# Performance work log

Hardware: AMD Instinct MI355X
Metric: run time of the kernel (lower is better)

## Reference

```python
import jax, jax.numpy as jnp
import numpy as np

B, S, C = 64, 256, 512
H, O, L = 1024, 1024, 4


def setup_inputs() -> dict:
    key = jax.random.key(0)
    ks = jax.random.split(key, 8)
    inp = {
        "x": jax.random.normal(ks[0], (B, S, C), dtype=jnp.float32),
        "hid_layer": jax.random.normal(ks[1], (B, L, H), dtype=jnp.float32),
        "fc1_w": jax.random.normal(ks[2], (H, H + C), dtype=jnp.float32) * (1.0 / np.sqrt(H + C)),
        "fc1_b": jax.random.normal(ks[3], (H,), dtype=jnp.float32) * 0.01,
        "fc2_w": jax.random.normal(ks[4], (O, H), dtype=jnp.float32) * (1.0 / np.sqrt(H)),
        "fc2_b": jax.random.normal(ks[5], (O,), dtype=jnp.float32) * 0.01,
        "lin_w": jax.random.normal(ks[6], (L - 1, H, H), dtype=jnp.float32) * (1.0 / np.sqrt(H)),
        "lin_b": jax.random.normal(ks[7], (L - 1, H), dtype=jnp.float32) * 0.01,
    }
    return inp


def reference(x, hid_layer, fc1_w, fc1_b, fc2_w, fc2_b, lin_w, lin_b):
    # x: [B,S,C] -> [S,B,C]; hid_layer: [B,L,H] -> [L,B,H]
    xs = jnp.transpose(x, (1, 0, 2))
    h = jnp.transpose(hid_layer, (1, 0, 2))
    h0 = h[0]          # layer-0 hidden: never updated in original code (constant)
    h_rest = h[1:]     # [L-1, B, H], evolves by repeated affine map
    n_inner = lin_w.shape[0]

    def step(carry, x_i):
        hr = carry  # [L-1, B, H]
        # hid_layer[i+1, j+1] = linears[j](hid_layer[i, j+1])
        h_new = jnp.einsum("lbh,lgh->lbg", hr, lin_w) + lin_b[:, None, :]
        xc = jnp.concatenate([x_i, h0], axis=1)            # [B, C+H]
        temp = jnp.tanh(xc @ fc1_w.T + fc1_b)              # [B, H]
        for j in range(n_inner):                           # static small loop
            temp = jnp.tanh(h_new[j] + temp)
        out = jax.nn.softmax(jax.nn.relu(temp @ fc2_w.T + fc2_b), axis=-1)
        return h_new, out

    _, outs = jax.lax.scan(step, h_rest, xs)
    return outs  # [S, B, O]
```

## Files before the change

### kernel.cpp

```cpp
#include <hip/hip_runtime.h>
#include <hip/hip_bf16.h>

#define Bn 64
#define Sn 256
#define Cn 512
#define Hn 1024
#define On 1024
#define NL 3

__global__ __launch_bounds__(256) void prep_kernel(const float* __restrict__ hid,
                                                   float* __restrict__ h0T) {
    __shared__ float T[64][65];
    int l = blockIdx.x >> 4;
    int kb = (blockIdx.x & 15) * 64;
    int tid = threadIdx.x;
    for (int e = tid; e < 1024; e += 256) {
        int b = e >> 4, k4 = (e & 15) * 4;
        float4 v = *(const float4*)&hid[(size_t)b * 4096 + (size_t)(l + 1) * 1024 + kb + k4];
        T[b][k4] = v.x; T[b][k4 + 1] = v.y; T[b][k4 + 2] = v.z; T[b][k4 + 3] = v.w;
    }
    __syncthreads();
    for (int e = tid; e < 1024; e += 256) {
        int k = e >> 4, b4 = (e & 15) * 4;
        float4 v = make_float4(T[b4][k], T[b4 + 1][k], T[b4 + 2][k], T[b4 + 3][k]);
        *(float4*)&h0T[(size_t)l * 65536 + (size_t)(kb + k) * 64 + b4] = v;
    }
}

__global__ __launch_bounds__(256) void g1_kernel(const float* __restrict__ hid,
                                                 const float* __restrict__ fc1_w,
                                                 const float* __restrict__ fc1_b,
                                                 float* __restrict__ h0proj) {
    __shared__ __align__(16) float h0s[Hn];
    int b = blockIdx.x;
    int tid = threadIdx.x;
    for (int i = tid; i < Hn; i += 256) h0s[i] = hid[(size_t)b * 4 * Hn + i];
    __syncthreads();
    for (int g = tid; g < Hn; g += 256) {
        const float* wr = fc1_w + (size_t)g * (Cn + Hn) + Cn;
        float acc = 0.f;
        for (int k = 0; k < Hn; k += 4) {
            float4 w4 = *(const float4*)&wr[k];
            acc = fmaf(w4.x, h0s[k + 0], acc);
            acc = fmaf(w4.y, h0s[k + 1], acc);
            acc = fmaf(w4.z, h0s[k + 2], acc);
            acc = fmaf(w4.w, h0s[k + 3], acc);
        }
        h0proj[b * Hn + g] = acc + fc1_b[g];
    }
}

__global__ __launch_bounds__(256) void g2_kernel(const float* __restrict__ x,
                                                 const float* __restrict__ fc1_w,
                                                 const float* __restrict__ h0proj,
                                                 __hip_bfloat16* __restrict__ tb) {
    __shared__ __align__(16) float As[64][64];
    __shared__ __align__(16) float Bs[64][64];
    int tid = threadIdx.x;
    int bx = blockIdx.x;
    int g0 = blockIdx.y * 64;
    int ml = tid & 63;
    int kq = tid >> 6;
    const float* xrow = x + (size_t)ml * (Sn * Cn) + (size_t)bx * Cn;
    const float* wrow = fc1_w + (size_t)(g0 + ml) * (Cn + Hn);
    int wave = tid >> 6, lane = tid & 63;
    int tm = (wave & 1) * 32 + (lane & 7) * 4;
    int tg = (wave >> 1) * 32 + (lane >> 3) * 4;
    float acc[4][4] = {};
    for (int kc = 0; kc < Cn / 64; ++kc) {
#pragma unroll
        for (int r = 0; r < 4; ++r) {
            int kk = kq * 16 + r * 4;
            float4 v = *(const float4*)&xrow[kc * 64 + kk];
            As[kk + 0][ml] = v.x; As[kk + 1][ml] = v.y;
            As[kk + 2][ml] = v.z; As[kk + 3][ml] = v.w;
        }
#pragma unroll
        for (int r = 0; r < 4; ++r) {
            int kk = kq * 16 + r * 4;
            float4 v = *(const float4*)&wrow[kc * 64 + kk];
            Bs[kk + 0][ml] = v.x; Bs[kk + 1][ml] = v.y;
            Bs[kk + 2][ml] = v.z; Bs[kk + 3][ml] = v.w;
        }
        __syncthreads();
#pragma unroll 4
        for (int k = 0; k < 64; ++k) {
            float4 a4 = *(const float4*)&As[k][tm];
            float4 b4 = *(const float4*)&Bs[k][tg];
            float av[4] = {a4.x, a4.y, a4.z, a4.w};
            float bv[4] = {b4.x, b4.y, b4.z, b4.w};
#pragma unroll
            for (int i = 0; i < 4; ++i)
#pragma unroll
                for (int j = 0; j < 4; ++j)
                    acc[i][j] = fmaf(av[i], bv[j], acc[i][j]);
        }
        __syncthreads();
    }
#pragma unroll
    for (int j = 0; j < 4; ++j) {
        int g = g0 + tg + j;
        union { ushort4 u4; __hip_bfloat16 h[4]; } cv;
#pragma unroll
        for (int i = 0; i < 4; ++i) {
            float hp = h0proj[(size_t)(tm + i) * Hn + g];
            cv.h[i] = __float2bfloat16(tanhf(acc[i][j] + hp));
        }
        *(ushort4*)&tb[((size_t)bx * Hn + g) * 64 + tm] = cv.u4;
    }
}

__global__ __launch_bounds__(256) void g3_kernel(const __hip_bfloat16* __restrict__ tb,
                                                 const float* __restrict__ fc2_w,
                                                 const float* __restrict__ fc2_b,
                                                 float* __restrict__ logits) {
    __shared__ __align__(16) float As[64][64];
    __shared__ __align__(16) float Bs[64][64];
    int tid = threadIdx.x;
    int bx = blockIdx.x;
    int g0 = blockIdx.y * 64;
    int ml = tid & 63;
    int kq = tid >> 6;
    const float* wrow = fc2_w + (size_t)(g0 + ml) * Hn;
    int wave = tid >> 6, lane = tid & 63;
    int tm = (wave & 1) * 32 + (lane & 7) * 4;
    int tg = (wave >> 1) * 32 + (lane >> 3) * 4;
    float acc[4][4] = {};
    for (int kc = 0; kc < Hn / 64; ++kc) {
        for (int e = tid; e < 4096; e += 256) {
            int kk = e >> 6, mm = e & 63;
            As[kk][mm] = __bfloat162float(tb[((size_t)bx * Hn + kc * 64 + kk) * 64 + mm]);
        }
#pragma unroll
        for (int r = 0; r < 4; ++r) {
            int kk = kq * 16 + r * 4;
            float4 v = *(const float4*)&wrow[kc * 64 + kk];
            Bs[kk + 0][ml] = v.x; Bs[kk + 1][ml] = v.y;
            Bs[kk + 2][ml] = v.z; Bs[kk + 3][ml] = v.w;
        }
        __syncthreads();
#pragma unroll 4
        for (int k = 0; k < 64; ++k) {
            float4 a4 = *(const float4*)&As[k][tm];
            float4 b4 = *(const float4*)&Bs[k][tg];
            float av[4] = {a4.x, a4.y, a4.z, a4.w};
            float bv[4] = {b4.x, b4.y, b4.z, b4.w};
#pragma unroll
            for (int i = 0; i < 4; ++i)
#pragma unroll
                for (int j = 0; j < 4; ++j)
                    acc[i][j] = fmaf(av[i], bv[j], acc[i][j]);
        }
        __syncthreads();
    }
    int m0 = bx * 64;
#pragma unroll
    for (int i = 0; i < 4; ++i) {
        int m = m0 + tm + i;
        float4 o;
        o.x = fmaxf(acc[i][0] + fc2_b[g0 + tg + 0], 0.f);
        o.y = fmaxf(acc[i][1] + fc2_b[g0 + tg + 1], 0.f);
        o.z = fmaxf(acc[i][2] + fc2_b[g0 + tg + 2], 0.f);
        o.w = fmaxf(acc[i][3] + fc2_b[g0 + tg + 3], 0.f);
        *(float4*)&logits[(size_t)m * Hn + g0 + tg] = o;
    }
}

__global__ __launch_bounds__(256) void cvec_kernel(const float* __restrict__ A,
                                                   const float* __restrict__ vecB,
                                                   const float* __restrict__ addB,
                                                   float* __restrict__ outv) {
    int row = blockIdx.x * 4 + (threadIdx.x >> 6);
    int lane = threadIdx.x & 63;
    int l = row >> 10;
    const float* ar = A + (size_t)row * Hn;
    const float* vb = vecB + (size_t)l * Hn;
    float s = 0.f;
#pragma unroll 4
    for (int j = 0; j < 16; ++j) {
        int k = lane + j * 64;
        s = fmaf(ar[k], vb[k], s);
    }
    s += __shfl_xor(s, 1);  s += __shfl_xor(s, 2);  s += __shfl_xor(s, 4);
    s += __shfl_xor(s, 8);  s += __shfl_xor(s, 16); s += __shfl_xor(s, 32);
    if (lane == 0) outv[row] = s + addB[row];
}

template<int NC>
__global__ __launch_bounds__(512, 2) void gsl4_kernel(
        const float* __restrict__ A,
        const float* __restrict__ Bsrc,
        unsigned long long bPanel, int bstride, int bcol0,
        float* __restrict__ dst, int dstride, int dcol0,
        const float* __restrict__ addRow,
        __hip_bfloat16* __restrict__ tb, const float* __restrict__ Xf,
        int folds, int do_gemm) {
    __shared__ __align__(16) float As[2][16][16];
    __shared__ __align__(16) float Xs[2][16][NC];
    const int tid = threadIdx.x;
    const int wg = blockIdx.x;
    const int row0 = wg * 16;
    const int l = row0 >> 10;

    if (folds >= 0) {
        for (int e = wg * 512 + tid; e < 4 * Hn * Bn; e += 192 * 512) {
            int b = e & 63, g = (e >> 6) & 1023, tp = e >> 16;
            int c = tp * 64 + b;
            size_t tix = ((size_t)(4 * folds + tp) * Hn + g) * 64 + b;
            float tv = __bfloat162float(tb[tix]);
            tv = tanhf(Xf[(size_t)g * 256 + c] + tv);
            tv = tanhf(Xf[262144 + (size_t)g * 256 + c] + tv);
            tv = tanhf(Xf[524288 + (size_t)g * 256 + c] + tv);
            tb[tix] = __float2bfloat16(tv);
        }
    }
    if (!do_gemm) return;

    const int cq = tid & 127;
    const int rq = tid >> 7;
    const float* __restrict__ Bp = Bsrc + (size_t)l * bPanel + bcol0;
    constexpr int NF4 = NC / 4;
    constexpr int TOT4 = 16 * NF4;
    constexpr int PFN = (TOT4 + 511) / 512;
    const bool cact = (2 * cq < NC);
    const int arow = tid & 15, akq = tid >> 4;
    const bool aact = (tid < 64);

    float acc[4][2] = {};
    float4 px[PFN];
    float4 pa;

#pragma unroll
    for (int i = 0; i < PFN; ++i) {
        int e = tid + i * 512;
        if ((TOT4 % 512 == 0) || e < TOT4) {
            int k = e / NF4, c4 = (e % NF4) * 4;
            px[i] = *(const float4*)(Bp + (size_t)k * bstride + c4);
        }
    }
    if (aact)
        pa = *(const float4*)(A + (size_t)(row0 + arow) * 1024 + akq * 4);
#pragma unroll
    for (int i = 0; i < PFN; ++i) {
        int e = tid + i * 512;
        if ((TOT4 % 512 == 0) || e < TOT4) {
            int k = e / NF4, c4 = (e % NF4) * 4;
            *(float4*)&Xs[0][k][c4] = px[i];
        }
    }
    if (aact) {
        As[0][akq * 4 + 0][arow] = pa.x;
        As[0][akq * 4 + 1][arow] = pa.y;
        As[0][akq * 4 + 2][arow] = pa.z;
        As[0][akq * 4 + 3][arow] = pa.w;
    }
    __syncthreads();

    for (int ck = 0; ck < 64; ++ck) {
        if (ck < 63) {
#pragma unroll
            for (int i = 0; i < PFN; ++i) {
                int e = tid + i * 512;
                if ((TOT4 % 512 == 0) || e < TOT4) {
                    int k = e / NF4, c4 = (e % NF4) * 4;
                    px[i] = *(const float4*)(Bp + (size_t)((ck + 1) * 16 + k) * bstride + c4);
                }
            }
            if (aact)
                pa = *(const float4*)(A + (size_t)(row0 + arow) * 1024 + (ck + 1) * 16 + akq * 4);
        }
        if (cact) {
            const float* xsc = &Xs[ck & 1][0][2 * cq];
            const float* asc = &As[ck & 1][0][rq * 4];
#pragma unroll
            for (int kk = 0; kk < 16; ++kk) {
                float4 a4 = *(const float4*)(asc + kk * 16);
                float2 x2 = *(const float2*)(xsc + kk * NC);
                acc[0][0] = fmaf(a4.x, x2.x, acc[0][0]);
                acc[0][1] = fmaf(a4.x, x2.y, acc[0][1]);
                acc[1][0] = fmaf(a4.y, x2.x, acc[1][0]);
                acc[1][1] = fmaf(a4.y, x2.y, acc[1][1]);
                acc[2][0] = fmaf(a4.z, x2.x, acc[2][0]);
                acc[2][1] = fmaf(a4.z, x2.y, acc[2][1]);
                acc[3][0] = fmaf(a4.w, x2.x, acc[3][0]);
                acc[3][1] = fmaf(a4.w, x2.y, acc[3][1]);
            }
        }
        if (ck < 63) {
#pragma unroll
            for (int i = 0; i < PFN; ++i) {
                int e = tid + i * 512;
                if ((TOT4 % 512 == 0) || e < TOT4) {
                    int k = e / NF4, c4 = (e % NF4) * 4;
                    *(float4*)&Xs[(ck + 1) & 1][k][c4] = px[i];
                }
            }
            if (aact) {
                As[(ck + 1) & 1][akq * 4 + 0][arow] = pa.x;
                As[(ck + 1) & 1][akq * 4 + 1][arow] = pa.y;
                As[(ck + 1) & 1][akq * 4 + 2][arow] = pa.z;
                As[(ck + 1) & 1][akq * 4 + 3][arow] = pa.w;
            }
            __syncthreads();
        }
    }

    if (cact) {
#pragma unroll
        for (int i = 0; i < 4; ++i) {
            int r = row0 + rq * 4 + i;
            float av = addRow ? addRow[r] : 0.0f;
            float2 o = make_float2(acc[i][0] + av, acc[i][1] + av);
            *(float2*)(dst + (size_t)r * dstride + dcol0 + 2 * cq) = o;
        }
    }
}

__global__ __launch_bounds__(256) void softmax_kernel(const float* __restrict__ logits,
                                                      float* __restrict__ out) {
    __shared__ float redm[4];
    __shared__ float reds[4];
    __shared__ float bcast[2];
    int row = blockIdx.x, tid = threadIdx.x;
    const float* in = logits + (size_t)row * On;
    float4 v = *(const float4*)&in[tid * 4];
    float mx = fmaxf(fmaxf(v.x, v.y), fmaxf(v.z, v.w));
#pragma unroll
    for (int o = 32; o > 0; o >>= 1) mx = fmaxf(mx, __shfl_down(mx, o));
    if ((tid & 63) == 0) redm[tid >> 6] = mx;
    __syncthreads();
    if (tid == 0) bcast[0] = fmaxf(fmaxf(redm[0], redm[1]), fmaxf(redm[2], redm[3]));
    __syncthreads();
    float M = bcast[0];
    float e0 = expf(v.x - M), e1 = expf(v.y - M), e2 = expf(v.z - M), e3 = expf(v.w - M);
    float s = e0 + e1 + e2 + e3;
#pragma unroll
    for (int o = 32; o > 0; o >>= 1) s += __shfl_down(s, o);
    if ((tid & 63) == 0) reds[tid >> 6] = s;
    __syncthreads();
    if (tid == 0) bcast[1] = reds[0] + reds[1] + reds[2] + reds[3];
    __syncthreads();
    float inv = 1.0f / bcast[1];
    float4 o4 = make_float4(e0 * inv, e1 * inv, e2 * inv, e3 * inv);
    *(float4*)&out[(size_t)row * On + tid * 4] = o4;
}

extern "C" void kernel_launch(void* const* d_in, const int* in_sizes, int n_in,
                              void* d_out, int out_size, void* d_ws, size_t ws_size,
                              hipStream_t stream) {
    const float* x     = (const float*)d_in[0];
    const float* hid   = (const float*)d_in[1];
    const float* fc1_w = (const float*)d_in[2];
    const float* fc1_b = (const float*)d_in[3];
    const float* fc2_w = (const float*)d_in[4];
    const float* fc2_b = (const float*)d_in[5];
    const float* lin_w = (const float*)d_in[6];
    const float* lin_b = (const float*)d_in[7];
    float* out = (float*)d_out;

    char* wsb = (char*)d_ws;
    __hip_bfloat16* tb = (__hip_bfloat16*)wsb;
    float* logits = (float*)(wsb + 33554432ull);
    float* w2     = (float*)(wsb + 100663296ull);
    float* w4     = (float*)(wsb + 113246208ull);
    float* X      = (float*)(wsb + 125829120ull);
    float* c2     = (float*)(wsb + 132120576ull);
    float* c4     = (float*)(wsb + 132132864ull);
    float* h0T    = (float*)(wsb + 132145152ull);
    float* h0proj = (float*)(wsb + 132931584ull);

    float* X0 = X;
    float* X1 = X + 786432;

    prep_kernel<<<48, 256, 0, stream>>>(hid, h0T);
    g1_kernel<<<Bn, 256, 0, stream>>>(hid, fc1_w, fc1_b, h0proj);
    g2_kernel<<<dim3(Sn, Hn / 64), 256, 0, stream>>>(x, fc1_w, h0proj, tb);

    cvec_kernel<<<768, 256, 0, stream>>>(lin_w, lin_b, lin_b, c2);
    for (int p = 0; p < 4; ++p)
        gsl4_kernel<256><<<192, 512, 0, stream>>>(lin_w, lin_w, 1048576ull, 1024, p * 256,
                                                  w2, 1024, p * 256, nullptr,
                                                  tb, nullptr, -1, 1);
    cvec_kernel<<<768, 256, 0, stream>>>(w2, c2, c2, c4);
    for (int p = 0; p < 4; ++p)
        gsl4_kernel<256><<<192, 512, 0, stream>>>(w2, w2, 1048576ull, 1024, p * 256,
                                                  w4, 1024, p * 256, nullptr,
                                                  tb, nullptr, -1, 1);
    gsl4_kernel<64><<<192, 512, 0, stream>>>(lin_w, h0T, 65536ull, 64, 0,
                                             X0, 256, 0, lin_b, tb, nullptr, -1, 1);
    gsl4_kernel<64><<<192, 512, 0, stream>>>(w2, h0T, 65536ull, 64, 0,
                                             X0, 256, 64, c2, tb, nullptr, -1, 1);
    gsl4_kernel<64><<<192, 512, 0, stream>>>(w4, h0T, 65536ull, 64, 0,
                                             X0, 256, 192, c4, tb, nullptr, -1, 1);
    gsl4_kernel<64><<<192, 512, 0, stream>>>(w2, X0, 262144ull, 256, 0,
                                             X0, 256, 128, c2, tb, nullptr, -1, 1);

    for (int s = 0; s < 63; ++s) {
        float* Xin  = (s & 1) ? X1 : X0;
        float* Xout = (s & 1) ? X0 : X1;
        gsl4_kernel<256><<<192, 512, 0, stream>>>(w4, Xin, 262144ull, 256, 0,
                                                  Xout, 256, 0, c4, tb, Xin, s, 1);
    }
    gsl4_kernel<256><<<192, 512, 0, stream>>>(w4, X1, 262144ull, 256, 0,
                                              X0, 256, 0, c4, tb, X1, 63, 0);

    g3_kernel<<<dim3(Sn, Hn / 64), 256, 0, stream>>>(tb, fc2_w, fc2_b, logits);
    softmax_kernel<<<Sn * Bn, 256, 0, stream>>>(logits, out);
}
```

Measured before the change: 5.034 ms.

## Fuse recurrence launches into one cooperative persistent kernel with grid syncs

The precompute GEMMs (W², W⁴, bias vectors, initial X panels) and the 63-step recurrence loop are merged into one cooperatively launched kernel of 192 blocks, with grid.sync between dependent phases. This replaces roughly eighty separate kernel launches and their launch gaps. The GEMM inner loop now uses two register prefetch buffers so loads run two chunks ahead instead of one. The cvec reduction is folded in per block. In exchange, grid-wide barriers now carry the dependencies, and every block must stay resident for the whole run.

```diff
diff --git a/kernel.cpp b/kernel.cpp
--- a/kernel.cpp
+++ b/kernel.cpp
@@ -1,5 +1,8 @@
 #include <hip/hip_runtime.h>
 #include <hip/hip_bf16.h>
+#include <hip/hip_cooperative_groups.h>
+
+namespace cg = cooperative_groups;
 
 #define Bn 64
 #define Sn 256
@@ -166,154 +169,177 @@
     }
 }
 
-__global__ __launch_bounds__(256) void cvec_kernel(const float* __restrict__ A,
-                                                   const float* __restrict__ vecB,
-                                                   const float* __restrict__ addB,
-                                                   float* __restrict__ outv) {
-    int row = blockIdx.x * 4 + (threadIdx.x >> 6);
-    int lane = threadIdx.x & 63;
-    int l = row >> 10;
-    const float* ar = A + (size_t)row * Hn;
-    const float* vb = vecB + (size_t)l * Hn;
-    float s = 0.f;
-#pragma unroll 4
-    for (int j = 0; j < 16; ++j) {
-        int k = lane + j * 64;
-        s = fmaf(ar[k], vb[k], s);
-    }
-    s += __shfl_xor(s, 1);  s += __shfl_xor(s, 2);  s += __shfl_xor(s, 4);
-    s += __shfl_xor(s, 8);  s += __shfl_xor(s, 16); s += __shfl_xor(s, 32);
-    if (lane == 0) outv[row] = s + addB[row];
-}
-
 template<int NC>
-__global__ __launch_bounds__(512, 2) void gsl4_kernel(
-        const float* __restrict__ A,
-        const float* __restrict__ Bsrc,
-        unsigned long long bPanel, int bstride, int bcol0,
+__device__ __forceinline__ void gemm_pass(
+        const float* __restrict__ A, int row0,
+        const float* __restrict__ Bp, int bstride,
         float* __restrict__ dst, int dstride, int dcol0,
-        const float* __restrict__ addRow,
-        __hip_bfloat16* __restrict__ tb, const float* __restrict__ Xf,
-        int folds, int do_gemm) {
-    __shared__ __align__(16) float As[2][16][16];
-    __shared__ __align__(16) float Xs[2][16][NC];
-    const int tid = threadIdx.x;
-    const int wg = blockIdx.x;
-    const int row0 = wg * 16;
-    const int l = row0 >> 10;
-
-    if (folds >= 0) {
-        for (int e = wg * 512 + tid; e < 4 * Hn * Bn; e += 192 * 512) {
-            int b = e & 63, g = (e >> 6) & 1023, tp = e >> 16;
-            int c = tp * 64 + b;
-            size_t tix = ((size_t)(4 * folds + tp) * Hn + g) * 64 + b;
-            float tv = __bfloat162float(tb[tix]);
-            tv = tanhf(Xf[(size_t)g * 256 + c] + tv);
-            tv = tanhf(Xf[262144 + (size_t)g * 256 + c] + tv);
-            tv = tanhf(Xf[524288 + (size_t)g * 256 + c] + tv);
-            tb[tix] = __float2bfloat16(tv);
-        }
-    }
-    if (!do_gemm) return;
-
-    const int cq = tid & 127;
-    const int rq = tid >> 7;
-    const float* __restrict__ Bp = Bsrc + (size_t)l * bPanel + bcol0;
+        const float* __restrict__ addRow, int tid,
+        float* __restrict__ AsF, float* __restrict__ XsF) {
     constexpr int NF4 = NC / 4;
     constexpr int TOT4 = 16 * NF4;
     constexpr int PFN = (TOT4 + 511) / 512;
+    const int cq = tid & 127;
+    const int rq = tid >> 7;
     const bool cact = (2 * cq < NC);
     const int arow = tid & 15, akq = tid >> 4;
     const bool aact = (tid < 64);
 
     float acc[4][2] = {};
-    float4 px[PFN];
-    float4 pa;
-
-#pragma unroll
-    for (int i = 0; i < PFN; ++i) {
-        int e = tid + i * 512;
-        if ((TOT4 % 512 == 0) || e < TOT4) {
-            int k = e / NF4, c4 = (e % NF4) * 4;
-            px[i] = *(const float4*)(Bp + (size_t)k * bstride + c4);
-        }
-    }
-    if (aact)
-        pa = *(const float4*)(A + (size_t)(row0 + arow) * 1024 + akq * 4);
-#pragma unroll
-    for (int i = 0; i < PFN; ++i) {
-        int e = tid + i * 512;
-        if ((TOT4 % 512 == 0) || e < TOT4) {
-            int k = e / NF4, c4 = (e % NF4) * 4;
-            *(float4*)&Xs[0][k][c4] = px[i];
-        }
-    }
-    if (aact) {
-        As[0][akq * 4 + 0][arow] = pa.x;
-        As[0][akq * 4 + 1][arow] = pa.y;
-        As[0][akq * 4 + 2][arow] = pa.z;
-        As[0][akq * 4 + 3][arow] = pa.w;
-    }
-    __syncthreads();
-
-    for (int ck = 0; ck < 64; ++ck) {
-        if (ck < 63) {
-#pragma unroll
-            for (int i = 0; i < PFN; ++i) {
-                int e = tid + i * 512;
-                if ((TOT4 % 512 == 0) || e < TOT4) {
-                    int k = e / NF4, c4 = (e % NF4) * 4;
-                    px[i] = *(const float4*)(Bp + (size_t)((ck + 1) * 16 + k) * bstride + c4);
-                }
+    float4 pxA[PFN], pxB[PFN], paA = {}, paB = {};
+
+    auto loadX = [&](int c, float4* px) {
+#pragma unroll
+        for (int i = 0; i < PFN; ++i) {
+            int e = tid + i * 512;
+            if ((TOT4 % 512 == 0) || e < TOT4) {
+                int k = e / NF4, c4 = (e % NF4) * 4;
+                px[i] = *(const float4*)(Bp + (size_t)(c * 16 + k) * bstride + c4);
             }
-            if (aact)
-                pa = *(const float4*)(A + (size_t)(row0 + arow) * 1024 + (ck + 1) * 16 + akq * 4);
-        }
-        if (cact) {
-            const float* xsc = &Xs[ck & 1][0][2 * cq];
-            const float* asc = &As[ck & 1][0][rq * 4];
-#pragma unroll
-            for (int kk = 0; kk < 16; ++kk) {
-                float4 a4 = *(const float4*)(asc + kk * 16);
-                float2 x2 = *(const float2*)(xsc + kk * NC);
-                acc[0][0] = fmaf(a4.x, x2.x, acc[0][0]);
-                acc[0][1] = fmaf(a4.x, x2.y, acc[0][1]);
-                acc[1][0] = fmaf(a4.y, x2.x, acc[1][0]);
-                acc[1][1] = fmaf(a4.y, x2.y, acc[1][1]);
-                acc[2][0] = fmaf(a4.z, x2.x, acc[2][0]);
-                acc[2][1] = fmaf(a4.z, x2.y, acc[2][1]);
-                acc[3][0] = fmaf(a4.w, x2.x, acc[3][0]);
-                acc[3][1] = fmaf(a4.w, x2.y, acc[3][1]);
+        }
+    };
+    auto writeX = [&](int c, const float4* px) {
+#pragma unroll
+        for (int i = 0; i < PFN; ++i) {
+            int e = tid + i * 512;
+            if ((TOT4 % 512 == 0) || e < TOT4) {
+                int k = e / NF4, c4 = (e % NF4) * 4;
+                *(float4*)&XsF[(size_t)(c & 1) * 4096 + k * 256 + c4] = px[i];
             }
         }
-        if (ck < 63) {
-#pragma unroll
-            for (int i = 0; i < PFN; ++i) {
-                int e = tid + i * 512;
-                if ((TOT4 % 512 == 0) || e < TOT4) {
-                    int k = e / NF4, c4 = (e % NF4) * 4;
-                    *(float4*)&Xs[(ck + 1) & 1][k][c4] = px[i];
-                }
-            }
-            if (aact) {
-                As[(ck + 1) & 1][akq * 4 + 0][arow] = pa.x;
-                As[(ck + 1) & 1][akq * 4 + 1][arow] = pa.y;
-                As[(ck + 1) & 1][akq * 4 + 2][arow] = pa.z;
-                As[(ck + 1) & 1][akq * 4 + 3][arow] = pa.w;
-            }
+    };
+    auto loadA = [&](int c) -> float4 {
+        return *(const float4*)(A + (size_t)(row0 + arow) * 1024 + c * 16 + akq * 4);
+    };
+    auto writeA = [&](int c, float4 pa) {
+        float* base = &AsF[(size_t)(c & 1) * 256 + arow];
+        base[(akq * 4 + 0) * 16] = pa.x;
+        base[(akq * 4 + 1) * 16] = pa.y;
+        base[(akq * 4 + 2) * 16] = pa.z;
+        base[(akq * 4 + 3) * 16] = pa.w;
+    };
+    auto compute = [&](int c) {
+        if (!cact) return;
+        const float* xsc = &XsF[(size_t)(c & 1) * 4096 + 2 * cq];
+        const float* asc = &AsF[(size_t)(c & 1) * 256 + rq * 4];
+#pragma unroll
+        for (int kk = 0; kk < 16; ++kk) {
+            float4 a4 = *(const float4*)(asc + kk * 16);
+            float2 x2 = *(const float2*)(xsc + kk * 256);
+            acc[0][0] = fmaf(a4.x, x2.x, acc[0][0]);
+            acc[0][1] = fmaf(a4.x, x2.y, acc[0][1]);
+            acc[1][0] = fmaf(a4.y, x2.x, acc[1][0]);
+            acc[1][1] = fmaf(a4.y, x2.y, acc[1][1]);
+            acc[2][0] = fmaf(a4.z, x2.x, acc[2][0]);
+            acc[2][1] = fmaf(a4.z, x2.y, acc[2][1]);
+            acc[3][0] = fmaf(a4.w, x2.x, acc[3][0]);
+            acc[3][1] = fmaf(a4.w, x2.y, acc[3][1]);
+        }
+    };
+
+    loadX(0, pxA); if (aact) paA = loadA(0);
+    loadX(1, pxB); if (aact) paB = loadA(1);
+    writeX(0, pxA); if (aact) writeA(0, paA);
+    __syncthreads();
+    for (int c2i = 0; c2i < 32; ++c2i) {
+        const int ck = 2 * c2i;
+        if (ck + 2 < 64) { loadX(ck + 2, pxA); if (aact) paA = loadA(ck + 2); }
+        compute(ck);
+        writeX(ck + 1, pxB); if (aact) writeA(ck + 1, paB);
+        __syncthreads();
+        if (ck + 3 < 64) { loadX(ck + 3, pxB); if (aact) paB = loadA(ck + 3); }
+        compute(ck + 1);
+        if (ck + 2 < 64) {
+            writeX(ck + 2, pxA); if (aact) writeA(ck + 2, paA);
             __syncthreads();
         }
     }
-
     if (cact) {
 #pragma unroll
         for (int i = 0; i < 4; ++i) {
             int r = row0 + rq * 4 + i;
             float av = addRow ? addRow[r] : 0.0f;
-            float2 o = make_float2(acc[i][0] + av, acc[i][1] + av);
-            *(float2*)(dst + (size_t)r * dstride + dcol0 + 2 * cq) = o;
-        }
-    }
+            *(float2*)(dst + (size_t)r * dstride + dcol0 + 2 * cq) =
+                make_float2(acc[i][0] + av, acc[i][1] + av);
+        }
+    }
+    __syncthreads();
+}
+
+__device__ __forceinline__ void cvec16(const float* __restrict__ A, int row0,
+                                       const float* __restrict__ vec,
+                                       const float* __restrict__ addv,
+                                       float* __restrict__ outv, int tid) {
+    int r = tid >> 5;
+    int seg = tid & 31;
+    const float* ar = A + (size_t)(row0 + r) * Hn;
+    float s = 0.f;
+#pragma unroll 8
+    for (int j = 0; j < 32; ++j) s = fmaf(ar[seg + j * 32], vec[seg + j * 32], s);
+    s += __shfl_xor(s, 1);  s += __shfl_xor(s, 2);  s += __shfl_xor(s, 4);
+    s += __shfl_xor(s, 8);  s += __shfl_xor(s, 16);
+    if (seg == 0) outv[row0 + r] = s + addv[row0 + r];
+}
+
+__device__ __forceinline__ void fold4(int s, const float* __restrict__ Xf,
+                                      __hip_bfloat16* __restrict__ tb, int wg, int tid) {
+    for (int e = wg * 512 + tid; e < 4 * Hn * Bn; e += 192 * 512) {
+        int b = e & 63, g = (e >> 6) & 1023, tp = e >> 16;
+        int c = tp * 64 + b;
+        size_t tix = ((size_t)(4 * s + tp) * Hn + g) * 64 + b;
+        float tv = __bfloat162float(tb[tix]);
+        tv = tanhf(Xf[(size_t)g * 256 + c] + tv);
+        tv = tanhf(Xf[262144 + (size_t)g * 256 + c] + tv);
+        tv = tanhf(Xf[524288 + (size_t)g * 256 + c] + tv);
+        tb[tix] = __float2bfloat16(tv);
+    }
+}
+
+__global__ __launch_bounds__(512, 2) void recur5_kernel(
+        const float* __restrict__ lin_w, const float* __restrict__ lin_b,
+        const float* __restrict__ h0T, __hip_bfloat16* __restrict__ tb,
+        float* __restrict__ w2, float* __restrict__ w4,
+        float* __restrict__ c2g, float* __restrict__ c4g,
+        float* __restrict__ X0, float* __restrict__ X1) {
+    __shared__ __align__(16) float AsF[512];
+    __shared__ __align__(16) float XsF[8192];
+    const int tid = threadIdx.x;
+    const int w = blockIdx.x;
+    const int row0 = w * 16;
+    const int l = row0 >> 10;
+    cg::grid_group grid = cg::this_grid();
+
+    cvec16(lin_w, row0, lin_b + l * Hn, lin_b, c2g, tid);
+    gemm_pass<64>(lin_w, row0, h0T + (size_t)l * 65536, 64,
+                  X0, 256, 0, lin_b, tid, AsF, XsF);
+    for (int p = 0; p < 4; ++p)
+        gemm_pass<256>(lin_w, row0, lin_w + (size_t)l * 1048576 + p * 256, 1024,
+                       w2, 1024, p * 256, nullptr, tid, AsF, XsF);
+    grid.sync();
+
+    cvec16(w2, row0, c2g + l * Hn, c2g, c4g, tid);
+    gemm_pass<64>(w2, row0, h0T + (size_t)l * 65536, 64,
+                  X0, 256, 64, c2g, tid, AsF, XsF);
+    for (int p = 0; p < 4; ++p)
+        gemm_pass<256>(w2, row0, w2 + (size_t)l * 1048576 + p * 256, 1024,
+                       w4, 1024, p * 256, nullptr, tid, AsF, XsF);
+    grid.sync();
+
+    gemm_pass<64>(w2, row0, X0 + (size_t)l * 262144, 256,
+                  X0, 256, 128, c2g, tid, AsF, XsF);
+    gemm_pass<64>(w4, row0, h0T + (size_t)l * 65536, 64,
+                  X0, 256, 192, c4g, tid, AsF, XsF);
+    grid.sync();
+
+    for (int s = 0; s < 63; ++s) {
+        const float* Xin = (s & 1) ? X1 : X0;
+        float* Xout = (s & 1) ? X0 : X1;
+        fold4(s, Xin, tb, w, tid);
+        gemm_pass<256>(w4, row0, Xin + (size_t)l * 262144, 256,
+                       Xout, 256, 0, c4g, tid, AsF, XsF);
+        grid.sync();
+    }
+    fold4(63, X1, tb, w, tid);
 }
 
 __global__ __launch_bounds__(256) void softmax_kernel(const float* __restrict__ logits,
@@ -376,33 +402,11 @@
     g1_kernel<<<Bn, 256, 0, stream>>>(hid, fc1_w, fc1_b, h0proj);
     g2_kernel<<<dim3(Sn, Hn / 64), 256, 0, stream>>>(x, fc1_w, h0proj, tb);
 
-    cvec_kernel<<<768, 256, 0, stream>>>(lin_w, lin_b, lin_b, c2);
-    for (int p = 0; p < 4; ++p)
-        gsl4_kernel<256><<<192, 512, 0, stream>>>(lin_w, lin_w, 1048576ull, 1024, p * 256,
-                                                  w2, 1024, p * 256, nullptr,
-                                                  tb, nullptr, -1, 1);
-    cvec_kernel<<<768, 256, 0, stream>>>(w2, c2, c2, c4);
-    for (int p = 0; p < 4; ++p)
-        gsl4_kernel<256><<<192, 512, 0, stream>>>(w2, w2, 1048576ull, 1024, p * 256,
-                                                  w4, 1024, p * 256, nullptr,
-                                                  tb, nullptr, -1, 1);
-    gsl4_kernel<64><<<192, 512, 0, stream>>>(lin_w, h0T, 65536ull, 64, 0,
-                                             X0, 256, 0, lin_b, tb, nullptr, -1, 1);
-    gsl4_kernel<64><<<192, 512, 0, stream>>>(w2, h0T, 65536ull, 64, 0,
-                                             X0, 256, 64, c2, tb, nullptr, -1, 1);
-    gsl4_kernel<64><<<192, 512, 0, stream>>>(w4, h0T, 65536ull, 64, 0,
-                                             X0, 256, 192, c4, tb, nullptr, -1, 1);
-    gsl4_kernel<64><<<192, 512, 0, stream>>>(w2, X0, 262144ull, 256, 0,
-                                             X0, 256, 128, c2, tb, nullptr, -1, 1);
-
-    for (int s = 0; s < 63; ++s) {
-        float* Xin  = (s & 1) ? X1 : X0;
-        float* Xout = (s & 1) ? X0 : X1;
-        gsl4_kernel<256><<<192, 512, 0, stream>>>(w4, Xin, 262144ull, 256, 0,
-                                                  Xout, 256, 0, c4, tb, Xin, s, 1);
-    }
-    gsl4_kernel<256><<<192, 512, 0, stream>>>(w4, X1, 262144ull, 256, 0,
-                                              X0, 256, 0, c4, tb, X1, 63, 0);
+    void* args[] = { (void*)&lin_w, (void*)&lin_b, (void*)&h0T, (void*)&tb,
+                     (void*)&w2, (void*)&w4, (void*)&c2, (void*)&c4,
+                     (void*)&X0, (void*)&X1 };
+    hipLaunchCooperativeKernel((const void*)recur5_kernel, dim3(192), dim3(512),
+                               args, 0, stream);
 
     g3_kernel<<<dim3(Sn, Hn / 64), 256, 0, stream>>>(tb, fc2_w, fc2_b, logits);
     softmax_kernel<<<Sn * Bn, 256, 0, stream>>>(logits, out);
```

After: 9.943 ms. 1.98x slower.

## Run recurrent W4 step GEMMs on bf16 MFMA with hi/lo split precision

Applied to the files above, without the earlier changes.

Replaces the fp32 FMA-based gsl4 step GEMM in the 63-step recurrence with an MFMA kernel. It splits W4 and the transposed state into bf16 hi+lo pairs and accumulates three bf16 products to approximate fp32 accuracy. The step kernel also writes the next state's transposed hi/lo split, so no separate conversion pass is needed between steps. This adds a one-time weight split, extra workspace buffers, and some loss of accuracy from dropping the lo*lo term.

```diff
diff --git a/kernel.cpp b/kernel.cpp
--- a/kernel.cpp
+++ b/kernel.cpp
@@ -7,6 +7,18 @@
 #define Hn 1024
 #define On 1024
 #define NL 3
+
+typedef __attribute__((ext_vector_type(8))) short bf16x8;
+typedef __attribute__((ext_vector_type(4))) float f32x4;
+
+__device__ __forceinline__ ushort f2bf(float x) {
+    __hip_bfloat16 b = __float2bfloat16(x);
+    return *(ushort*)&b;
+}
+__device__ __forceinline__ float bf2f(ushort u) {
+    __hip_bfloat16 b = *(__hip_bfloat16*)&u;
+    return __bfloat162float(b);
+}
 
 __global__ __launch_bounds__(256) void prep_kernel(const float* __restrict__ hid,
                                                    float* __restrict__ h0T) {
@@ -188,34 +200,16 @@
 
 template<int NC>
 __global__ __launch_bounds__(512, 2) void gsl4_kernel(
-        const float* __restrict__ A,
-        const float* __restrict__ Bsrc,
+        const float* __restrict__ A, const float* __restrict__ Bsrc,
         unsigned long long bPanel, int bstride, int bcol0,
         float* __restrict__ dst, int dstride, int dcol0,
-        const float* __restrict__ addRow,
-        __hip_bfloat16* __restrict__ tb, const float* __restrict__ Xf,
-        int folds, int do_gemm) {
+        const float* __restrict__ addRow) {
     __shared__ __align__(16) float As[2][16][16];
     __shared__ __align__(16) float Xs[2][16][NC];
     const int tid = threadIdx.x;
     const int wg = blockIdx.x;
     const int row0 = wg * 16;
     const int l = row0 >> 10;
-
-    if (folds >= 0) {
-        for (int e = wg * 512 + tid; e < 4 * Hn * Bn; e += 192 * 512) {
-            int b = e & 63, g = (e >> 6) & 1023, tp = e >> 16;
-            int c = tp * 64 + b;
-            size_t tix = ((size_t)(4 * folds + tp) * Hn + g) * 64 + b;
-            float tv = __bfloat162float(tb[tix]);
-            tv = tanhf(Xf[(size_t)g * 256 + c] + tv);
-            tv = tanhf(Xf[262144 + (size_t)g * 256 + c] + tv);
-            tv = tanhf(Xf[524288 + (size_t)g * 256 + c] + tv);
-            tb[tix] = __float2bfloat16(tv);
-        }
-    }
-    if (!do_gemm) return;
-
     const int cq = tid & 127;
     const int rq = tid >> 7;
     const float* __restrict__ Bp = Bsrc + (size_t)l * bPanel + bcol0;
@@ -238,8 +232,7 @@
             px[i] = *(const float4*)(Bp + (size_t)k * bstride + c4);
         }
     }
-    if (aact)
-        pa = *(const float4*)(A + (size_t)(row0 + arow) * 1024 + akq * 4);
+    if (aact) pa = *(const float4*)(A + (size_t)(row0 + arow) * 1024 + akq * 4);
 #pragma unroll
     for (int i = 0; i < PFN; ++i) {
         int e = tid + i * 512;
@@ -316,6 +309,194 @@
     }
 }
 
+__global__ __launch_bounds__(256) void wsplit_kernel(const float* __restrict__ w4,
+                                                     ushort* __restrict__ whi,
+                                                     ushort* __restrict__ wlo) {
+    int i = blockIdx.x * 256 + threadIdx.x;
+    float4 v = ((const float4*)w4)[i];
+    ushort4 h, l;
+    h.x = f2bf(v.x); l.x = f2bf(v.x - bf2f(h.x));
+    h.y = f2bf(v.y); l.y = f2bf(v.y - bf2f(h.y));
+    h.z = f2bf(v.z); l.z = f2bf(v.z - bf2f(h.z));
+    h.w = f2bf(v.w); l.w = f2bf(v.w - bf2f(h.w));
+    *(ushort4*)&whi[(size_t)i * 4] = h;
+    *(ushort4*)&wlo[(size_t)i * 4] = l;
+}
+
+__global__ __launch_bounds__(256) void xsplitT_kernel(const float* __restrict__ X0,
+                                                      ushort* __restrict__ xthi,
+                                                      ushort* __restrict__ xtlo) {
+    __shared__ float T[64][65];
+    int bid = blockIdx.x;
+    int l = bid >> 6;
+    int rem = bid & 63;
+    int gb = rem >> 2, cbk = rem & 3;
+    int g0 = gb * 64, c0 = cbk * 64;
+    int tid = threadIdx.x;
+#pragma unroll
+    for (int p = 0; p < 4; ++p) {
+        int g = p * 16 + (tid >> 4);
+        int c4 = (tid & 15) * 4;
+        float4 v = *(const float4*)&X0[(size_t)l * 262144 + (size_t)(g0 + g) * 256 + c0 + c4];
+        T[g][c4] = v.x; T[g][c4 + 1] = v.y; T[g][c4 + 2] = v.z; T[g][c4 + 3] = v.w;
+    }
+    __syncthreads();
+#pragma unroll
+    for (int p = 0; p < 4; ++p) {
+        int c = p * 16 + (tid >> 4);
+        int k4 = (tid & 15) * 4;
+        ushort4 h, lo;
+        float v0 = T[k4 + 0][c], v1 = T[k4 + 1][c], v2 = T[k4 + 2][c], v3 = T[k4 + 3][c];
+        h.x = f2bf(v0); lo.x = f2bf(v0 - bf2f(h.x));
+        h.y = f2bf(v1); lo.y = f2bf(v1 - bf2f(h.y));
+        h.z = f2bf(v2); lo.z = f2bf(v2 - bf2f(h.z));
+        h.w = f2bf(v3); lo.w = f2bf(v3 - bf2f(h.w));
+        size_t off = (size_t)l * 262144 + (size_t)(c0 + c) * 1024 + g0 + k4;
+        *(ushort4*)&xthi[off] = h;
+        *(ushort4*)&xtlo[off] = lo;
+    }
+}
+
+__global__ __launch_bounds__(256) void msl_kernel(
+        const ushort* __restrict__ Whi, const ushort* __restrict__ Wlo,
+        const ushort* __restrict__ BThi, const ushort* __restrict__ BTlo,
+        const float* __restrict__ c4,
+        const float* __restrict__ Xin, float* __restrict__ Xout,
+        ushort* __restrict__ XThiOut, ushort* __restrict__ XTloOut,
+        __hip_bfloat16* __restrict__ tb, int s) {
+    __shared__ __align__(16) ushort Ah[4096];
+    __shared__ __align__(16) ushort Al[4096];
+    __shared__ __align__(16) ushort Bh[4096];
+    __shared__ __align__(16) ushort Bl[4096];
+    const int tid = threadIdx.x;
+    const int rb = blockIdx.x;
+    const int cb = blockIdx.y;
+    const int row0 = rb * 64;
+    const int col0 = cb * 64;
+    const int l = rb >> 4;
+
+    {
+        int wg = rb * 4 + cb;
+        for (int e = wg * 256 + tid; e < 4 * Hn * Bn; e += 192 * 256) {
+            int b = e & 63, g = (e >> 6) & 1023, tp = e >> 16;
+            int c = tp * 64 + b;
+            size_t tix = ((size_t)(4 * s + tp) * Hn + g) * 64 + b;
+            float tv = __bfloat162float(tb[tix]);
+            tv = tanhf(Xin[(size_t)g * 256 + c] + tv);
+            tv = tanhf(Xin[262144 + (size_t)g * 256 + c] + tv);
+            tv = tanhf(Xin[524288 + (size_t)g * 256 + c] + tv);
+            tb[tix] = __float2bfloat16(tv);
+        }
+    }
+
+    const int lane = tid & 63;
+    const int w = tid >> 6;
+    const int fr = lane & 15;
+    const int fq = lane >> 4;
+
+    f32x4 acc[4];
+#pragma unroll
+    for (int i = 0; i < 4; ++i) acc[i] = (f32x4){0.f, 0.f, 0.f, 0.f};
+
+    const int srow = tid >> 3;
+    const int sk16 = (tid & 7) * 8;
+
+    const ushort* Ahsrc = Whi + (size_t)row0 * 1024;
+    const ushort* Alsrc = Wlo + (size_t)row0 * 1024;
+    const ushort* Bhsrc = BThi + (size_t)l * 262144 + (size_t)col0 * 1024;
+    const ushort* Blsrc = BTlo + (size_t)l * 262144 + (size_t)col0 * 1024;
+
+    float4 pf0[4], pf1[4];
+
+    auto issue = [&](int k0) {
+        size_t g0o = (size_t)srow * 1024 + k0 + sk16;
+        size_t g1o = (size_t)(srow + 32) * 1024 + k0 + sk16;
+        pf0[0] = *(const float4*)(Ahsrc + g0o);
+        pf0[1] = *(const float4*)(Alsrc + g0o);
+        pf0[2] = *(const float4*)(Bhsrc + g0o);
+        pf0[3] = *(const float4*)(Blsrc + g0o);
+        pf1[0] = *(const float4*)(Ahsrc + g1o);
+        pf1[1] = *(const float4*)(Alsrc + g1o);
+        pf1[2] = *(const float4*)(Bhsrc + g1o);
+        pf1[3] = *(const float4*)(Blsrc + g1o);
+    };
+    auto commit = [&]() {
+        int off0 = srow * 64 + (sk16 ^ ((srow & 7) << 3));
+        int off1 = (srow + 32) * 64 + (sk16 ^ (((srow + 32) & 7) << 3));
+        *(float4*)(Ah + off0) = pf0[0];
+        *(float4*)(Al + off0) = pf0[1];
+        *(float4*)(Bh + off0) = pf0[2];
+        *(float4*)(Bl + off0) = pf0[3];
+        *(float4*)(Ah + off1) = pf1[0];
+        *(float4*)(Al + off1) = pf1[1];
+        *(float4*)(Bh + off1) = pf1[2];
+        *(float4*)(Bl + off1) = pf1[3];
+    };
+
+    issue(0);
+    commit();
+    __syncthreads();
+    for (int ck = 0; ck < 16; ++ck) {
+        if (ck < 15) issue((ck + 1) * 64);
+#pragma unroll
+        for (int ks = 0; ks < 2; ++ks) {
+            int k16 = ks * 32 + fq * 8;
+            int bro = w * 16 + fr;
+            int boff = bro * 64 + (k16 ^ ((bro & 7) << 3));
+            bf16x8 bhf = *(const bf16x8*)(Bh + boff);
+            bf16x8 blf = *(const bf16x8*)(Bl + boff);
+#pragma unroll
+            for (int rt = 0; rt < 4; ++rt) {
+                int aro = rt * 16 + fr;
+                int aoff = aro * 64 + (k16 ^ ((aro & 7) << 3));
+                bf16x8 ahf = *(const bf16x8*)(Ah + aoff);
+                bf16x8 alf = *(const bf16x8*)(Al + aoff);
+                acc[rt] = __builtin_amdgcn_mfma_f32_16x16x32_bf16(ahf, bhf, acc[rt], 0, 0, 0);
+                acc[rt] = __builtin_amdgcn_mfma_f32_16x16x32_bf16(ahf, blf, acc[rt], 0, 0, 0);
+                acc[rt] = __builtin_amdgcn_mfma_f32_16x16x32_bf16(alf, bhf, acc[rt], 0, 0, 0);
+            }
+        }
+        __syncthreads();
+        if (ck < 15) {
+            commit();
+            __syncthreads();
+        }
+    }
+
+    int cg = col0 + w * 16 + fr;
+#pragma unroll
+    for (int rt = 0; rt < 4; ++rt) {
+        int rbase = row0 + rt * 16 + fq * 4;
+        float hv[4];
+        ushort hi[4], lo[4];
+#pragma unroll
+        for (int r = 0; r < 4; ++r) {
+            hv[r] = acc[rt][r] + c4[rbase + r];
+            Xout[(size_t)(rbase + r) * 256 + cg] = hv[r];
+            hi[r] = f2bf(hv[r]);
+            lo[r] = f2bf(hv[r] - bf2f(hi[r]));
+        }
+        int rloc = rbase - l * 1024;
+        size_t toff = (size_t)l * 262144 + (size_t)cg * 1024 + rloc;
+        *(ushort4*)&XThiOut[toff] = make_ushort4(hi[0], hi[1], hi[2], hi[3]);
+        *(ushort4*)&XTloOut[toff] = make_ushort4(lo[0], lo[1], lo[2], lo[3]);
+    }
+}
+
+__global__ __launch_bounds__(256) void foldb_kernel(const float* __restrict__ Xf,
+                                                    __hip_bfloat16* __restrict__ tb, int s) {
+    for (int e = blockIdx.x * 256 + threadIdx.x; e < 4 * Hn * Bn; e += gridDim.x * 256) {
+        int b = e & 63, g = (e >> 6) & 1023, tp = e >> 16;
+        int c = tp * 64 + b;
+        size_t tix = ((size_t)(4 * s + tp) * Hn + g) * 64 + b;
+        float tv = __bfloat162float(tb[tix]);
+        tv = tanhf(Xf[(size_t)g * 256 + c] + tv);
+        tv = tanhf(Xf[262144 + (size_t)g * 256 + c] + tv);
+        tv = tanhf(Xf[524288 + (size_t)g * 256 + c] + tv);
+        tb[tix] = __float2bfloat16(tv);
+    }
+}
+
 __global__ __launch_bounds__(256) void softmax_kernel(const float* __restrict__ logits,
                                                       float* __restrict__ out) {
     __shared__ float redm[4];
@@ -360,18 +541,22 @@
 
     char* wsb = (char*)d_ws;
     __hip_bfloat16* tb = (__hip_bfloat16*)wsb;
+    ushort* W4hi  = (ushort*)(wsb + 33554432ull);
+    ushort* W4lo  = (ushort*)(wsb + 39845888ull);
+    ushort* XThi0 = (ushort*)(wsb + 46137344ull);
+    ushort* XTlo0 = (ushort*)(wsb + 47710208ull);
+    ushort* XThi1 = (ushort*)(wsb + 49283072ull);
+    ushort* XTlo1 = (ushort*)(wsb + 50855936ull);
     float* logits = (float*)(wsb + 33554432ull);
     float* w2     = (float*)(wsb + 100663296ull);
     float* w4     = (float*)(wsb + 113246208ull);
-    float* X      = (float*)(wsb + 125829120ull);
+    float* X0     = (float*)(wsb + 125829120ull);
+    float* X1     = (float*)(wsb + 128974848ull);
     float* c2     = (float*)(wsb + 132120576ull);
     float* c4     = (float*)(wsb + 132132864ull);
     float* h0T    = (float*)(wsb + 132145152ull);
     float* h0proj = (float*)(wsb + 132931584ull);
 
-    float* X0 = X;
-    float* X1 = X + 786432;
-
     prep_kernel<<<48, 256, 0, stream>>>(hid, h0T);
     g1_kernel<<<Bn, 256, 0, stream>>>(hid, fc1_w, fc1_b, h0proj);
     g2_kernel<<<dim3(Sn, Hn / 64), 256, 0, stream>>>(x, fc1_w, h0proj, tb);
@@ -379,30 +564,34 @@
     cvec_kernel<<<768, 256, 0, stream>>>(lin_w, lin_b, lin_b, c2);
     for (int p = 0; p < 4; ++p)
         gsl4_kernel<256><<<192, 512, 0, stream>>>(lin_w, lin_w, 1048576ull, 1024, p * 256,
-                                                  w2, 1024, p * 256, nullptr,
-                                                  tb, nullptr, -1, 1);
+                                                  w2, 1024, p * 256, nullptr);
     cvec_kernel<<<768, 256, 0, stream>>>(w2, c2, c2, c4);
     for (int p = 0; p < 4; ++p)
         gsl4_kernel<256><<<192, 512, 0, stream>>>(w2, w2, 1048576ull, 1024, p * 256,
-                                                  w4, 1024, p * 256, nullptr,
-                                                  tb, nullptr, -1, 1);
+                                                  w4, 1024, p * 256, nullptr);
     gsl4_kernel<64><<<192, 512, 0, stream>>>(lin_w, h0T, 65536ull, 64, 0,
-                                             X0, 256, 0, lin_b, tb, nullptr, -1, 1);
+                                             X0, 256, 0, lin_b);
     gsl4_kernel<64><<<192, 512, 0, stream>>>(w2, h0T, 65536ull, 64, 0,
-                                             X0, 256, 64, c2, tb, nullptr, -1, 1);
+                                             X0, 256, 64, c2);
     gsl4_kernel<64><<<192, 512, 0, stream>>>(w4, h0T, 65536ull, 64, 0,
-                                             X0, 256, 192, c4, tb, nullptr, -1, 1);
+                                             X0, 256, 192, c4);
     gsl4_kernel<64><<<192, 512, 0, stream>>>(w2, X0, 262144ull, 256, 0,
-                                             X0, 256, 128, c2, tb, nullptr, -1, 1);
+                                             X0, 256, 128, c2);
+
+    wsplit_kernel<<<3072, 256, 0, stream>>>(w4, W4hi, W4lo);
+    xsplitT_kernel<<<192, 256, 0, stream>>>(X0, XThi0, XTlo0);
 
     for (int s = 0; s < 63; ++s) {
-        float* Xin  = (s & 1) ? X1 : X0;
-        float* Xout = (s & 1) ? X0 : X1;
-        gsl4_kernel<256><<<192, 512, 0, stream>>>(w4, Xin, 262144ull, 256, 0,
-                                                  Xout, 256, 0, c4, tb, Xin, s, 1);
-    }
-    gsl4_kernel<256><<<192, 512, 0, stream>>>(w4, X1, 262144ull, 256, 0,
-                                              X0, 256, 0, c4, tb, X1, 63, 0);
+        const float* Xi = (s & 1) ? X1 : X0;
+        float* Xo       = (s & 1) ? X0 : X1;
+        const ushort* Bhi = (s & 1) ? XThi1 : XThi0;
+        const ushort* Blo = (s & 1) ? XTlo1 : XTlo0;
+        ushort* Bho = (s & 1) ? XThi0 : XThi1;
+        ushort* Blo2 = (s & 1) ? XTlo0 : XTlo1;
+        msl_kernel<<<dim3(48, 4), 256, 0, stream>>>(W4hi, W4lo, Bhi, Blo, c4,
+                                                    Xi, Xo, Bho, Blo2, tb, s);
+    }
+    foldb_kernel<<<512, 256, 0, stream>>>(X1, tb, 63);
 
     g3_kernel<<<dim3(Sn, Hn / 64), 256, 0, stream>>>(tb, fc2_w, fc2_b, logits);
     softmax_kernel<<<Sn * Bn, 256, 0, stream>>>(logits, out);
```

After: 6.170 ms. 22.6% more time.
